# Optimization experiments

Measured on AMD Instinct MI355X. Metric: run time of the kernel, lower is better.

## Reference

```python
import jax, jax.numpy as jnp
import numpy as np

BETA = 0.9
THRESH = 1.0
SLOPE = 50.0

@jax.custom_vjp
def spike(x):
    # heaviside with fast_sigmoid(slope=50) surrogate gradient
    return (x > 0).astype(x.dtype)

def _spike_fwd(x):
    return spike(x), x

def _spike_bwd(x, g):
    grad = g / (SLOPE * jnp.abs(x) + 1.0) ** 2
    return (grad,)

spike.defvjp(_spike_fwd, _spike_bwd)

def setup_inputs() -> dict:
    key = jax.random.key(0)
    ks = jax.random.split(key, 9)
    T, B, D, H, C = 100, 128, 2048, 2048, 100
    s_in, s_h = 1.0 / np.sqrt(D), 1.0 / np.sqrt(H)
    return {
        'x_seq': jax.random.normal(ks[0], (T, B, D), dtype=jnp.float32),
        'W1': jax.random.uniform(ks[1], (D, H), minval=-s_in, maxval=s_in, dtype=jnp.float32),
        'b1': jax.random.uniform(ks[2], (H,), minval=-s_in, maxval=s_in, dtype=jnp.float32),
        'W2': jax.random.uniform(ks[3], (H, H), minval=-s_h, maxval=s_h, dtype=jnp.float32),
        'b2': jax.random.uniform(ks[4], (H,), minval=-s_h, maxval=s_h, dtype=jnp.float32),
        'W3': jax.random.uniform(ks[5], (H, H), minval=-s_h, maxval=s_h, dtype=jnp.float32),
        'b3': jax.random.uniform(ks[6], (H,), minval=-s_h, maxval=s_h, dtype=jnp.float32),
        'Wo': jax.random.uniform(ks[7], (H, C), minval=-s_h, maxval=s_h, dtype=jnp.float32),
        'bo': jax.random.uniform(ks[8], (C,), minval=-s_h, maxval=s_h, dtype=jnp.float32),
    }

def _lif(cur, mem):
    # snntorch Leaky (reset-by-subtraction): reset uses previous membrane
    reset = (mem - THRESH > 0).astype(mem.dtype)
    mem_new = BETA * mem + cur - reset * THRESH
    spk = spike(mem_new - THRESH)
    return spk, mem_new

def reference(x_seq, W1, b1, W2, b2, W3, b3, Wo, bo):
    T, B, _ = x_seq.shape
    H = W1.shape[1]
    C = Wo.shape[1]
    mem0 = (jnp.zeros((B, H)), jnp.zeros((B, H)), jnp.zeros((B, H)), jnp.zeros((B, C)))
    spk_sum0 = jnp.zeros((B, C))

    def step(carry, x_t):
        (m1, m2, m3, mo), ssum = carry
        s1, m1 = _lif(x_t @ W1 + b1, m1)
        s2, m2 = _lif(s1 @ W2 + b2, m2)
        s3, m3 = _lif(s2 @ W3 + b3, m3)
        so, mo = _lif(s3 @ Wo + bo, mo)
        return ((m1, m2, m3, mo), ssum + so), None

    (_, spk_out_sum), _ = jax.lax.scan(step, (mem0, spk_sum0), x_seq)
    return spk_out_sum
```

## Files before the change

### kernel.cpp

```cpp
#include <hip/hip_runtime.h>

typedef short short8 __attribute__((ext_vector_type(8)));
typedef float f32x4 __attribute__((ext_vector_type(4)));
typedef int int4v __attribute__((ext_vector_type(4)));

#define TT 100
#define BB 128
#define HH 2048
#define CC 100
#define NBLK 256
#define CHUNK 10
#define NCH (TT / CHUNK)
#define NPHASE (NCH + 3)
#define SLOTW 8192

__device__ inline unsigned short f2bf(float f) {
  unsigned u = __float_as_uint(f);
  return (unsigned short)((u + 0x7FFF + ((u >> 16) & 1)) >> 16);
}
__device__ inline float bf2f(unsigned short b) {
  return __uint_as_float((unsigned)b << 16);
}

__global__ __launch_bounds__(256) void transpose_cvt(
    const float* __restrict__ W, unsigned short* __restrict__ Wt)
{
  __shared__ float t[32][33];
  int n0 = blockIdx.x * 32, k0 = blockIdx.y * 32;
  int tx = threadIdx.x, ty = threadIdx.y;
  #pragma unroll
  for (int j = 0; j < 4; ++j)
    t[ty + 8 * j][tx] = W[(size_t)(k0 + ty + 8 * j) * HH + n0 + tx];
  __syncthreads();
  #pragma unroll
  for (int j = 0; j < 4; ++j)
    Wt[(size_t)(n0 + ty + 8 * j) * HH + k0 + tx] = f2bf(t[tx][ty + 8 * j]);
}

__global__ __launch_bounds__(512) void cvt_x(
    const float* __restrict__ x, unsigned short* __restrict__ xb, long n8)
{
  long i = (long)blockIdx.x * blockDim.x + threadIdx.x;
  if (i >= n8) return;
  const float4* p = (const float4*)x + i * 2;
  float4 a = p[0], b = p[1];
  short8 pv;
  pv[0] = (short)f2bf(a.x); pv[1] = (short)f2bf(a.y);
  pv[2] = (short)f2bf(a.z); pv[3] = (short)f2bf(a.w);
  pv[4] = (short)f2bf(b.x); pv[5] = (short)f2bf(b.y);
  pv[6] = (short)f2bf(b.z); pv[7] = (short)f2bf(b.w);
  *(short8*)(xb + i * 8) = pv;
}

__global__ __launch_bounds__(256) void gemm_big_bf16(
    const unsigned short* __restrict__ Ab, const unsigned short* __restrict__ Wt,
    const float* __restrict__ bias, unsigned short* __restrict__ cur)
{
  __shared__ unsigned short As[128 * 128];
  __shared__ unsigned short Bs[64 * 128];
  const int tid = threadIdx.x;
  const int w = tid >> 6, l = tid & 63;
  const int wm = w & 1, wn = w >> 1;
  const int c16 = l & 15, g = l >> 4;
  const int n0 = blockIdx.x * 64, m0 = blockIdx.y * 128;
  f32x4 acc[4][2] = {};

  for (int k0 = 0; k0 < 2048; k0 += 128) {
    #pragma unroll
    for (int i = 0; i < 8; ++i) {
      int gg = tid + i * 256;
      int r = gg >> 4, gi = gg & 15;
      int kb = (gi * 16) ^ ((r & 7) << 4);
      const char* src = (const char*)(Ab + (size_t)(m0 + r) * HH + k0) + kb;
      *(int4v*)((char*)As + r * 256 + kb) = *(const int4v*)src;
    }
    #pragma unroll
    for (int i = 0; i < 4; ++i) {
      int gg = tid + i * 256;
      int r = gg >> 4, gi = gg & 15;
      int kb = (gi * 16) ^ ((r & 7) << 4);
      const char* bsrc = (const char*)(Wt + (size_t)(n0 + r) * HH + k0) + kb;
      *(int4v*)((char*)Bs + r * 256 + kb) = *(const int4v*)bsrc;
    }
    __syncthreads();
    #pragma unroll
    for (int kk = 0; kk < 4; ++kk) {
      int koff = (kk * 4 + g) * 16;
      short8 a[4], b[2];
      #pragma unroll
      for (int mi = 0; mi < 4; ++mi) {
        int mr = wm * 64 + mi * 16 + c16;
        a[mi] = *(short8*)((char*)As + mr * 256 + (koff ^ ((mr & 7) << 4)));
      }
      #pragma unroll
      for (int ni = 0; ni < 2; ++ni) {
        int nr = wn * 32 + ni * 16 + c16;
        b[ni] = *(short8*)((char*)Bs + nr * 256 + (koff ^ ((nr & 7) << 4)));
      }
      #pragma unroll
      for (int mi = 0; mi < 4; ++mi)
        #pragma unroll
        for (int ni = 0; ni < 2; ++ni)
          acc[mi][ni] = __builtin_amdgcn_mfma_f32_16x16x32_bf16(
              a[mi], b[ni], acc[mi][ni], 0, 0, 0);
    }
    __syncthreads();
  }
  #pragma unroll
  for (int mi = 0; mi < 4; ++mi)
    #pragma unroll
    for (int ni = 0; ni < 2; ++ni) {
      int col = n0 + wn * 32 + ni * 16 + c16;
      int rbase = m0 + wm * 64 + mi * 16 + g * 4;
      float bv = bias[col];
      #pragma unroll
      for (int j = 0; j < 4; ++j)
        cur[(size_t)(rbase + j) * HH + col] = f2bf(acc[mi][ni][j] + bv);
    }
}

__global__ __launch_bounds__(256) void gemm_big_f32(
    const float* __restrict__ A, const unsigned short* __restrict__ Wt,
    const float* __restrict__ bias, unsigned short* __restrict__ cur)
{
  __shared__ unsigned short As[128 * 128];
  __shared__ unsigned short Bs[64 * 128];
  const int tid = threadIdx.x;
  const int w = tid >> 6, l = tid & 63;
  const int wm = w & 1, wn = w >> 1;
  const int c16 = l & 15, g = l >> 4;
  const int n0 = blockIdx.x * 64, m0 = blockIdx.y * 128;
  f32x4 acc[4][2] = {};

  for (int k0 = 0; k0 < 2048; k0 += 128) {
    #pragma unroll
    for (int i = 0; i < 8; ++i) {
      int gg = tid + i * 256;
      int r = gg >> 4, gi = gg & 15;
      int kb = (gi * 16) ^ ((r & 7) << 4);
      const float* src = A + (size_t)(m0 + r) * HH + k0 + (kb >> 1);
      float4 f0 = *(const float4*)src, f1 = *(const float4*)(src + 4);
      short8 pv;
      pv[0] = (short)f2bf(f0.x); pv[1] = (short)f2bf(f0.y);
      pv[2] = (short)f2bf(f0.z); pv[3] = (short)f2bf(f0.w);
      pv[4] = (short)f2bf(f1.x); pv[5] = (short)f2bf(f1.y);
      pv[6] = (short)f2bf(f1.z); pv[7] = (short)f2bf(f1.w);
      *(int4v*)((char*)As + r * 256 + kb) = *(int4v*)&pv;
    }
    #pragma unroll
    for (int i = 0; i < 4; ++i) {
      int gg = tid + i * 256;
      int r = gg >> 4, gi = gg & 15;
      int kb = (gi * 16) ^ ((r & 7) << 4);
      const char* bsrc = (const char*)(Wt + (size_t)(n0 + r) * HH + k0) + kb;
      *(int4v*)((char*)Bs + r * 256 + kb) = *(const int4v*)bsrc;
    }
    __syncthreads();
    #pragma unroll
    for (int kk = 0; kk < 4; ++kk) {
      int koff = (kk * 4 + g) * 16;
      short8 a[4], b[2];
      #pragma unroll
      for (int mi = 0; mi < 4; ++mi) {
        int mr = wm * 64 + mi * 16 + c16;
        a[mi] = *(short8*)((char*)As + mr * 256 + (koff ^ ((mr & 7) << 4)));
      }
      #pragma unroll
      for (int ni = 0; ni < 2; ++ni) {
        int nr = wn * 32 + ni * 16 + c16;
        b[ni] = *(short8*)((char*)Bs + nr * 256 + (koff ^ ((nr & 7) << 4)));
      }
      #pragma unroll
      for (int mi = 0; mi < 4; ++mi)
        #pragma unroll
        for (int ni = 0; ni < 2; ++ni)
          acc[mi][ni] = __builtin_amdgcn_mfma_f32_16x16x32_bf16(
              a[mi], b[ni], acc[mi][ni], 0, 0, 0);
    }
    __syncthreads();
  }
  #pragma unroll
  for (int mi = 0; mi < 4; ++mi)
    #pragma unroll
    for (int ni = 0; ni < 2; ++ni) {
      int col = n0 + wn * 32 + ni * 16 + c16;
      int rbase = m0 + wm * 64 + mi * 16 + g * 4;
      float bv = bias[col];
      #pragma unroll
      for (int j = 0; j < 4; ++j)
        cur[(size_t)(rbase + j) * HH + col] = f2bf(acc[mi][ni][j] + bv);
    }
}

__global__ void init_kernel(unsigned* flags, int n)
{
  int i = blockIdx.x * blockDim.x + threadIdx.x;
  int stride = gridDim.x * blockDim.x;
  for (int j = i; j < n; j += stride) flags[j] = 0u;
}

__global__ __launch_bounds__(512) void snn_persist(
    const unsigned short* __restrict__ cur1,
    const float* __restrict__ W2, const float* __restrict__ b2,
    const float* __restrict__ W3, const float* __restrict__ b3,
    const float* __restrict__ Wo, const float* __restrict__ bo,
    unsigned* __restrict__ s1b, unsigned* __restrict__ s2b,
    unsigned* __restrict__ s3b,
    float* __restrict__ outsum, unsigned* __restrict__ flags,
    unsigned* __restrict__ go)
{
  __shared__ int4v sred[6 * 256];
  __shared__ unsigned sow[CHUNK * 64];
  __shared__ unsigned long long swm[CHUNK];
  __shared__ float smax[16][33];
  __shared__ float sscale[16];
  __shared__ float srscale[16];

  const int blk = blockIdx.x, tid = threadIdx.x;
  const int w = tid >> 6, l = tid & 63;
  const int km = w >> 1, wm = w & 1;
  const int c16 = l & 15, g = l >> 4;
  const bool isL2 = blk < 128;
  const int panel = blk & 127;
  const int n0c = panel * 16;
  const float* Wsrc = isL2 ? W2 : W3;
  const float* bias = isL2 ? b2 : b3;
  const int col = n0c + c16;

  float mx = 0.f;
  for (int s = 0; s < 8; ++s) {
    int kb = km * 512 + s * 64 + g * 16;
    #pragma unroll
    for (int e = 0; e < 16; ++e)
      mx = fmaxf(mx, fabsf(Wsrc[(size_t)(kb + e) * HH + col]));
  }
  smax[c16][w * 4 + g] = mx;
  __syncthreads();
  if (tid < 16) {
    float m = 0.f;
    #pragma unroll
    for (int i = 0; i < 32; ++i) m = fmaxf(m, smax[tid][i]);
    sscale[tid] = m * (1.f / 127.f);
    srscale[tid] = (m > 0.f) ? (127.f / m) : 0.f;
  }
  __syncthreads();
  const float scl = sscale[c16], rsc = srscale[c16];
  const float bv = bias[col];

  int4v Breg[8];
  for (int s = 0; s < 8; ++s) {
    int4v q = {0, 0, 0, 0};
    int kb = km * 512 + s * 64 + g * 16;
    #pragma unroll
    for (int e = 0; e < 16; ++e) {
      float v = Wsrc[(size_t)(kb + e) * HH + col];
      int qi = (int)rintf(v * rsc);
      qi = qi > 127 ? 127 : (qi < -127 ? -127 : qi);
      q[e >> 2] |= (qi & 0xFF) << ((e & 3) * 8);
    }
    Breg[s] = q;
  }

  int ppos;
  {
    int wv = panel >> 1;
    ppos = ((wv >> 4) << 5) + ((wv & 1) << 4) + ((wv & 15) >> 1) +
           ((panel & 1) << 3);
  }

  f32x4 m1reg = {0.f, 0.f, 0.f, 0.f};
  f32x4 memb[4] = {};
  float memo = 0.f, osumo = 0.f;
  const float boc = (!isL2 && tid < CC) ? bo[tid] : 0.f;
  const int rowa = wm * 64 + c16;

  for (int p = 0; p < NPHASE; ++p) {
    if (isL2 && p < NCH) {
      unsigned cw0[CHUNK], cw1[CHUNK];
      #pragma unroll
      for (int st = 0; st < CHUNK; ++st) {
        const unsigned* cp = (const unsigned*)(cur1 +
            ((size_t)(p * CHUNK + st) * BB + blk) * HH) + tid * 2;
        cw0[st] = cp[0]; cw1[st] = cp[1];
      }
      #pragma unroll
      for (int st = 0; st < CHUNK; ++st) {
        float cv[4] = { bf2f((unsigned short)(cw0[st] & 0xFFFF)),
                        bf2f((unsigned short)(cw0[st] >> 16)),
                        bf2f((unsigned short)(cw1[st] & 0xFFFF)),
                        bf2f((unsigned short)(cw1[st] >> 16)) };
        unsigned nib = 0;
        #pragma unroll
        for (int j = 0; j < 4; ++j) {
          float mo = m1reg[j];
          float mn = 0.9f * mo + cv[j] - ((mo > 1.f) ? 1.f : 0.f);
          m1reg[j] = mn;
          nib |= (mn > 1.f ? 1u : 0u) << j;
        }
        unsigned v = nib;
        v |= ((unsigned)__shfl_xor((int)v, 1)) << 4;
        v |= ((unsigned)__shfl_xor((int)v, 2)) << 8;
        v |= ((unsigned)__shfl_xor((int)v, 4)) << 16;
        if ((tid & 7) == 0) {
          int w8 = tid >> 3;
          int q0 = ((w8 >> 4) << 5) + ((w8 & 1) << 4) + ((w8 & 15) >> 1);
          unsigned short* so = (unsigned short*)(s1b +
              (size_t)(p * CHUNK + st) * SLOTW) + blk * 128;
          so[q0] = (unsigned short)(v & 0xFFFF);
          so[q0 + 8] = (unsigned short)(v >> 16);
        }
      }
    }

    int tch = p - (isL2 ? 1 : 2);
    if (tch >= 0 && tch < NCH) {
      const unsigned* sinb = isL2 ? s1b : s2b;
      unsigned* soutb = isL2 ? s2b : s3b;
      int4v A0[4], A1[4];
      {
        const char* sb = (const char*)(sinb + (size_t)(tch * CHUNK) * SLOTW);
        #pragma unroll
        for (int mi = 0; mi < 4; ++mi)
          A0[mi] = *(const int4v*)(sb + (rowa + mi * 16) * 256 + km * 64 + g * 16);
      }
      #pragma unroll 2
      for (int st = 0; st < CHUNK; ++st) {
        const int t = tch * CHUNK + st;
        int4v* Ac = (st & 1) ? A1 : A0;
        int4v* An = (st & 1) ? A0 : A1;
        if (st < CHUNK - 1) {
          const char* sb = (const char*)(sinb + (size_t)(t + 1) * SLOTW);
          #pragma unroll
          for (int mi = 0; mi < 4; ++mi)
            An[mi] = *(const int4v*)(sb + (rowa + mi * 16) * 256 + km * 64 + g * 16);
        }
        int4v acc[4] = {};
        #pragma unroll
        for (int s = 0; s < 8; ++s)
          #pragma unroll
          for (int mi = 0; mi < 4; ++mi) {
            unsigned word = (unsigned)Ac[mi][s >> 1];
            unsigned h = (s & 1) ? (word >> 16) : (word & 0xFFFFu);
            int4v af;
            af[0] = (int)(((h & 15u) * 0x204081u) & 0x01010101u);
            af[1] = (int)((((h >> 4) & 15u) * 0x204081u) & 0x01010101u);
            af[2] = (int)((((h >> 8) & 15u) * 0x204081u) & 0x01010101u);
            af[3] = (int)(((h >> 12) * 0x204081u) & 0x01010101u);
            acc[mi] = __builtin_amdgcn_mfma_i32_16x16x64_i8(
                af, Breg[s], acc[mi], 0, 0, 0);
          }
        __syncthreads();
        if (km > 0) {
          #pragma unroll
          for (int mi = 0; mi < 4; ++mi)
            sred[((km - 1) * 2 + wm) * 256 + mi * 64 + l] = acc[mi];
        }
        __syncthreads();
        if (km == 0) {
          #pragma unroll
          for (int mi = 0; mi < 4; ++mi) {
            int4v tot = acc[mi];
            #pragma unroll
            for (int r = 0; r < 3; ++r)
              tot = tot + sred[(r * 2 + wm) * 256 + mi * 64 + l];
            unsigned long long bal[4];
            #pragma unroll
            for (int j = 0; j < 4; ++j) {
              float curv = (float)tot[j] * scl + bv;
              float mo = memb[mi][j];
              float mn = 0.9f * mo + curv - ((mo > 1.f) ? 1.f : 0.f);
              memb[mi][j] = mn;
              bal[j] = __ballot((int)(mn > 1.f));
            }
            if (c16 == 0) {
              unsigned short* so = (unsigned short*)(soutb + (size_t)t * SLOTW);
              #pragma unroll
              for (int j = 0; j < 4; ++j) {
                int row = wm * 64 + mi * 16 + g * 4 + j;
                so[row * 128 + ppos] =
                    (unsigned short)((bal[j] >> (g * 16)) & 0xFFFFull);
              }
            }
          }
        }
      }
    }

    int oc = p - 3;
    if (!isL2 && oc >= 0 && oc < NCH) {
      int r = blk - 128;
      for (int i = tid; i < CHUNK * 64; i += 512)
        sow[i] = s3b[(size_t)(oc * CHUNK + (i >> 6)) * SLOTW + r * 64 + (i & 63)];
      __syncthreads();
      if (tid < CHUNK) {
        unsigned long long m = 0;
        for (int wd = 0; wd < 64; ++wd)
          if (sow[tid * 64 + wd]) m |= 1ull << wd;
        swm[tid] = m;
      }
      __syncthreads();
      if (tid < CC) {
        #pragma unroll 1
        for (int st = 0; st < CHUNK; ++st) {
          float curv = boc;
          unsigned long long m = swm[st];
          while (m) {
            int wd = (int)__ffsll((long long)m) - 1; m &= m - 1;
            unsigned wv2 = sow[st * 64 + wd];
            #pragma unroll
            for (int hf = 0; hf < 2; ++hf) {
              unsigned hv = hf ? (wv2 >> 16) : (wv2 & 0xFFFFu);
              int P = wd * 2 + hf;
              int kap = ((P >> 5) << 5) + ((P & 7) << 2) + ((P >> 3) & 3);
              while (hv) {
                int b = (int)__ffs(hv) - 1; hv &= hv - 1;
                curv += Wo[(size_t)(kap * 16 + b) * CC + tid];
              }
            }
          }
          float mo = memo;
          float mn = 0.9f * mo + curv - ((mo > 1.f) ? 1.f : 0.f);
          memo = mn;
          if (mn > 1.f) osumo += 1.f;
        }
      }
    }

    if (p < NPHASE - 1) {
      unsigned gen = (unsigned)(p + 1);
      __syncthreads();
      if (tid == 0)
        __hip_atomic_store(&flags[blk * 32], gen, __ATOMIC_RELEASE,
                           __HIP_MEMORY_SCOPE_AGENT);
      if (blk == 0) {
        if (tid < NBLK) {
          int guard = 0;
          while (__hip_atomic_load(&flags[tid * 32], __ATOMIC_ACQUIRE,
                                   __HIP_MEMORY_SCOPE_AGENT) < gen) {
            __builtin_amdgcn_s_sleep(2);
            if (++guard > (1 << 22)) break;
          }
        }
        __syncthreads();
        if (tid == 0)
          __hip_atomic_store(go, gen, __ATOMIC_RELEASE,
                             __HIP_MEMORY_SCOPE_AGENT);
      } else {
        if (tid == 0) {
          int guard = 0;
          while (__hip_atomic_load(go, __ATOMIC_ACQUIRE,
                                   __HIP_MEMORY_SCOPE_AGENT) < gen) {
            __builtin_amdgcn_s_sleep(4);
            if (++guard > (1 << 22)) break;
          }
        }
        __syncthreads();
      }
    }
  }

  if (!isL2 && tid < CC)
    outsum[(blk - 128) * CC + tid] = osumo;
}

extern "C" void kernel_launch(void* const* d_in, const int* in_sizes, int n_in,
                              void* d_out, int out_size, void* d_ws, size_t ws_size,
                              hipStream_t stream)
{
  const float* x  = (const float*)d_in[0];
  const float* W1 = (const float*)d_in[1];
  const float* b1 = (const float*)d_in[2];
  const float* W2 = (const float*)d_in[3];
  const float* b2 = (const float*)d_in[4];
  const float* W3 = (const float*)d_in[5];
  const float* b3 = (const float*)d_in[6];
  const float* Wo = (const float*)d_in[7];
  const float* bo = (const float*)d_in[8];
  float* out = (float*)d_out;

  unsigned* flags = (unsigned*)d_ws;
  unsigned* go = flags + 8192;
  unsigned* s1b = flags + 16384;
  unsigned* s2b = s1b + (size_t)TT * SLOTW;
  unsigned* s3b = s2b + (size_t)TT * SLOTW;
  unsigned short* Wt1 = (unsigned short*)(s3b + (size_t)TT * SLOTW);
  unsigned short* cur1 = Wt1 + (size_t)HH * HH;
  unsigned short* xb = cur1 + (size_t)TT * BB * HH;
  size_t need_xb = (size_t)((char*)(xb + (size_t)TT * BB * HH) - (char*)d_ws);

  hipLaunchKernelGGL(init_kernel, dim3(32), dim3(256), 0, stream, flags, 16384);
  hipLaunchKernelGGL(transpose_cvt, dim3(64, 64), dim3(32, 8), 0, stream, W1, Wt1);
  if (ws_size >= need_xb) {
    long n8 = (long)TT * BB * HH / 8;
    hipLaunchKernelGGL(cvt_x, dim3((unsigned)((n8 + 511) / 512)), dim3(512),
                       0, stream, x, xb, n8);
    hipLaunchKernelGGL(gemm_big_bf16, dim3(HH / 64, (TT * BB) / 128), dim3(256),
                       0, stream, xb, Wt1, b1, cur1);
  } else {
    hipLaunchKernelGGL(gemm_big_f32, dim3(HH / 64, (TT * BB) / 128), dim3(256),
                       0, stream, x, Wt1, b1, cur1);
  }
  hipLaunchKernelGGL(snn_persist, dim3(NBLK), dim3(512), 0, stream,
                     cur1, W2, b2, W3, b3, Wo, bo,
                     s1b, s2b, s3b, out, flags, go);
}
```

Baseline: 855.8 us.

## Give each wave the full K range to drop cross-wave reduction syncs

Changes the work split in the persistent layer-2/3 kernel. Each of the 8 waves now owns 16 batch rows and the full K=2048 reduction, holding all 32 int8 weight fragments in registers, where before work was split four ways along K and reduced through shared memory behind two __syncthreads per timestep. This removes the LDS reduction and barriers on the serial per-timestep critical path, and the per-column scale is computed with wave shuffles instead of shared memory. In exchange register pressure rises sharply (Breg grows to 32 int4 vectors, with launch bounds set to one block per SM), each wave runs a longer dependent MFMA accumulation chain, and the spike word packing order (ppos) changes to match.

```diff
diff --git a/kernel.cpp b/kernel.cpp
--- a/kernel.cpp
+++ b/kernel.cpp
@@ -199,7 +199,7 @@
   for (int j = i; j < n; j += stride) flags[j] = 0u;
 }
 
-__global__ __launch_bounds__(512) void snn_persist(
+__global__ __launch_bounds__(512, 1) void snn_persist(
     const unsigned short* __restrict__ cur1,
     const float* __restrict__ W2, const float* __restrict__ b2,
     const float* __restrict__ W3, const float* __restrict__ b3,
@@ -209,16 +209,11 @@
     float* __restrict__ outsum, unsigned* __restrict__ flags,
     unsigned* __restrict__ go)
 {
-  __shared__ int4v sred[6 * 256];
   __shared__ unsigned sow[CHUNK * 64];
   __shared__ unsigned long long swm[CHUNK];
-  __shared__ float smax[16][33];
-  __shared__ float sscale[16];
-  __shared__ float srscale[16];
 
   const int blk = blockIdx.x, tid = threadIdx.x;
   const int w = tid >> 6, l = tid & 63;
-  const int km = w >> 1, wm = w & 1;
   const int c16 = l & 15, g = l >> 4;
   const bool isL2 = blk < 128;
   const int panel = blk & 127;
@@ -228,29 +223,23 @@
   const int col = n0c + c16;
 
   float mx = 0.f;
-  for (int s = 0; s < 8; ++s) {
-    int kb = km * 512 + s * 64 + g * 16;
+  for (int s = 0; s < 32; ++s) {
+    int kb = s * 64 + g * 16;
     #pragma unroll
     for (int e = 0; e < 16; ++e)
       mx = fmaxf(mx, fabsf(Wsrc[(size_t)(kb + e) * HH + col]));
   }
-  smax[c16][w * 4 + g] = mx;
-  __syncthreads();
-  if (tid < 16) {
-    float m = 0.f;
-    #pragma unroll
-    for (int i = 0; i < 32; ++i) m = fmaxf(m, smax[tid][i]);
-    sscale[tid] = m * (1.f / 127.f);
-    srscale[tid] = (m > 0.f) ? (127.f / m) : 0.f;
-  }
-  __syncthreads();
-  const float scl = sscale[c16], rsc = srscale[c16];
+  mx = fmaxf(mx, __shfl_xor(mx, 16));
+  mx = fmaxf(mx, __shfl_xor(mx, 32));
+  const float scl = mx * (1.f / 127.f);
+  const float rsc = (mx > 0.f) ? (127.f / mx) : 0.f;
   const float bv = bias[col];
 
-  int4v Breg[8];
-  for (int s = 0; s < 8; ++s) {
+  int4v Breg[32];
+  #pragma unroll 4
+  for (int s = 0; s < 32; ++s) {
     int4v q = {0, 0, 0, 0};
-    int kb = km * 512 + s * 64 + g * 16;
+    int kb = s * 64 + g * 16;
     #pragma unroll
     for (int e = 0; e < 16; ++e) {
       float v = Wsrc[(size_t)(kb + e) * HH + col];
@@ -261,18 +250,14 @@
     Breg[s] = q;
   }
 
-  int ppos;
-  {
-    int wv = panel >> 1;
-    ppos = ((wv >> 4) << 5) + ((wv & 1) << 4) + ((wv & 15) >> 1) +
-           ((panel & 1) << 3);
-  }
+  const int ppos = ((panel >> 5) << 5) + ((panel & 3) << 3) + ((panel >> 2) & 7);
+  const int arow = w * 16 + c16;
+  const int abyte = arow * 256 + g * 16;
 
   f32x4 m1reg = {0.f, 0.f, 0.f, 0.f};
-  f32x4 memb[4] = {};
+  f32x4 memb = {0.f, 0.f, 0.f, 0.f};
   float memo = 0.f, osumo = 0.f;
   const float boc = (!isL2 && tid < CC) ? bo[tid] : 0.f;
-  const int rowa = wm * 64 + c16;
 
   for (int p = 0; p < NPHASE; ++p) {
     if (isL2 && p < NCH) {
@@ -320,8 +305,8 @@
       {
         const char* sb = (const char*)(sinb + (size_t)(tch * CHUNK) * SLOTW);
         #pragma unroll
-        for (int mi = 0; mi < 4; ++mi)
-          A0[mi] = *(const int4v*)(sb + (rowa + mi * 16) * 256 + km * 64 + g * 16);
+        for (int ch = 0; ch < 4; ++ch)
+          A0[ch] = *(const int4v*)(sb + abyte + ch * 64);
       }
       #pragma unroll 2
       for (int st = 0; st < CHUNK; ++st) {
@@ -331,56 +316,40 @@
         if (st < CHUNK - 1) {
           const char* sb = (const char*)(sinb + (size_t)(t + 1) * SLOTW);
           #pragma unroll
-          for (int mi = 0; mi < 4; ++mi)
-            An[mi] = *(const int4v*)(sb + (rowa + mi * 16) * 256 + km * 64 + g * 16);
-        }
-        int4v acc[4] = {};
-        #pragma unroll
-        for (int s = 0; s < 8; ++s)
+          for (int ch = 0; ch < 4; ++ch)
+            An[ch] = *(const int4v*)(sb + abyte + ch * 64);
+        }
+        int4v acc = {0, 0, 0, 0};
+        #pragma unroll
+        for (int ch = 0; ch < 4; ++ch)
           #pragma unroll
-          for (int mi = 0; mi < 4; ++mi) {
-            unsigned word = (unsigned)Ac[mi][s >> 1];
-            unsigned h = (s & 1) ? (word >> 16) : (word & 0xFFFFu);
+          for (int ss = 0; ss < 8; ++ss) {
+            unsigned word = (unsigned)Ac[ch][ss >> 1];
+            unsigned h = (ss & 1) ? (word >> 16) : (word & 0xFFFFu);
             int4v af;
             af[0] = (int)(((h & 15u) * 0x204081u) & 0x01010101u);
             af[1] = (int)((((h >> 4) & 15u) * 0x204081u) & 0x01010101u);
             af[2] = (int)((((h >> 8) & 15u) * 0x204081u) & 0x01010101u);
             af[3] = (int)(((h >> 12) * 0x204081u) & 0x01010101u);
-            acc[mi] = __builtin_amdgcn_mfma_i32_16x16x64_i8(
-                af, Breg[s], acc[mi], 0, 0, 0);
+            acc = __builtin_amdgcn_mfma_i32_16x16x64_i8(
+                af, Breg[ch * 8 + ss], acc, 0, 0, 0);
           }
-        __syncthreads();
-        if (km > 0) {
+        unsigned long long bal[4];
+        #pragma unroll
+        for (int j = 0; j < 4; ++j) {
+          float curv = (float)acc[j] * scl + bv;
+          float mo = memb[j];
+          float mn = 0.9f * mo + curv - ((mo > 1.f) ? 1.f : 0.f);
+          memb[j] = mn;
+          bal[j] = __ballot((int)(mn > 1.f));
+        }
+        if (c16 == 0) {
+          unsigned short* so = (unsigned short*)(soutb + (size_t)t * SLOTW);
           #pragma unroll
-          for (int mi = 0; mi < 4; ++mi)
-            sred[((km - 1) * 2 + wm) * 256 + mi * 64 + l] = acc[mi];
-        }
-        __syncthreads();
-        if (km == 0) {
-          #pragma unroll
-          for (int mi = 0; mi < 4; ++mi) {
-            int4v tot = acc[mi];
-            #pragma unroll
-            for (int r = 0; r < 3; ++r)
-              tot = tot + sred[(r * 2 + wm) * 256 + mi * 64 + l];
-            unsigned long long bal[4];
-            #pragma unroll
-            for (int j = 0; j < 4; ++j) {
-              float curv = (float)tot[j] * scl + bv;
-              float mo = memb[mi][j];
-              float mn = 0.9f * mo + curv - ((mo > 1.f) ? 1.f : 0.f);
-              memb[mi][j] = mn;
-              bal[j] = __ballot((int)(mn > 1.f));
-            }
-            if (c16 == 0) {
-              unsigned short* so = (unsigned short*)(soutb + (size_t)t * SLOTW);
-              #pragma unroll
-              for (int j = 0; j < 4; ++j) {
-                int row = wm * 64 + mi * 16 + g * 4 + j;
-                so[row * 128 + ppos] =
-                    (unsigned short)((bal[j] >> (g * 16)) & 0xFFFFull);
-              }
-            }
+          for (int j = 0; j < 4; ++j) {
+            int row = w * 16 + g * 4 + j;
+            so[row * 128 + ppos] =
+                (unsigned short)((bal[j] >> (g * 16)) & 0xFFFFull);
           }
         }
       }
@@ -424,6 +393,7 @@
           if (mn > 1.f) osumo += 1.f;
         }
       }
+      __syncthreads();
     }
 
     if (p < NPHASE - 1) {
```

Result: slower. 969.2 us (+13.2%).
